# Kernel tuning notes

Hardware: AMD Instinct MI355X
Metric: run time of the kernel (lower is better)

The kernel has to match this reference:

```python
import jax, jax.numpy as jnp
import numpy as np

E = 1024  # embed_dim
H = 16    # num_heads
D = E // H  # head_dim


def setup_inputs() -> dict:
    key = jax.random.key(0)
    ks = jax.random.split(key, 9)
    s = 0.02
    return {
        "hidden_state": jax.random.normal(ks[0], (4, 1024, E), jnp.float32),
        "Wq": jax.random.normal(ks[1], (H, D, E), jnp.float32) * s,
        "bq": jax.random.normal(ks[2], (H, D), jnp.float32) * s,
        "Wk": jax.random.normal(ks[3], (H, D, E), jnp.float32) * s,
        "bk": jax.random.normal(ks[4], (H, D), jnp.float32) * s,
        "Wv": jax.random.normal(ks[5], (H, D, E), jnp.float32) * s,
        "bv": jax.random.normal(ks[6], (H, D), jnp.float32) * s,
        "Wo": jax.random.normal(ks[7], (E, E), jnp.float32) * s,
        "bo": jax.random.normal(ks[8], (E,), jnp.float32) * s,
    }


def _mha(x, Wq, bq, Wk, bk, Wv, bv, Wo, bo):
    # Per-head linear projections (torch Linear: y = x W^T + b), batched over heads.
    q = jnp.einsum("bse,hde->bhsd", x, Wq) + bq[None, :, None, :]
    k = jnp.einsum("bse,hde->bhsd", x, Wk) + bk[None, :, None, :]
    v = jnp.einsum("bse,hde->bhsd", x, Wv) + bv[None, :, None, :]
    scores = jnp.einsum("bhsd,bhtd->bhst", q, k) / jnp.sqrt(jnp.asarray(D, x.dtype))
    w = jax.nn.softmax(scores, axis=-1)  # F.softmax default -> last dim
    o = jnp.einsum("bhst,bhtd->bhsd", w, v)
    # concat heads along last dim: [B,S,H*D] in head order (matches torch.cat)
    B, _, S, _ = o.shape
    o = jnp.transpose(o, (0, 2, 1, 3)).reshape(B, S, H * D)
    return o @ Wo.T + bo


def reference(hidden_state, Wq, bq, Wk, bk, Wv, bv, Wo, bo):
    return _mha(hidden_state, Wq, bq, Wk, bk, Wv, bv, Wo, bo)
```

## Files before the change

### kernel.cpp

```cpp
#include <hip/hip_runtime.h>
#include <hip/hip_bf16.h>
#include <stdint.h>

#define E_DIM 1024
#define H_NUM 16
#define D_DIM 64
#define B_NUM 4
#define S_LEN 1024

typedef __attribute__((ext_vector_type(8))) short bf16x8;
typedef __attribute__((ext_vector_type(4))) short bf16x4;
typedef __attribute__((ext_vector_type(4))) float f32x4;

#define SOFTMAX_C2 0.18033688011112042f

__device__ inline ushort f2b(float x) {
    __hip_bfloat16 h = __float2bfloat16(x);
    return *(ushort*)&h;
}
__device__ inline float b2f(ushort u) {
    __hip_bfloat16 h = *(__hip_bfloat16*)&u;
    return __bfloat162float(h);
}
__device__ inline uint pk2(float a, float b) {
    __hip_bfloat162 h = __float22bfloat162_rn(make_float2(a, b));
    return *(uint*)&h;
}
__device__ inline float fexp2(float x) { return __builtin_amdgcn_exp2f(x); }

__device__ inline void gld16(const ushort* g, ushort* l) {
    __builtin_amdgcn_global_load_lds((const __attribute__((address_space(1))) void*)g,
                                     (__attribute__((address_space(3))) void*)l, 16, 0, 0);
}

__global__ __launch_bounds__(256)
void convert_all(const float* __restrict__ X,  const float* __restrict__ Wq,
                 const float* __restrict__ Wk, const float* __restrict__ Wv,
                 const float* __restrict__ Wo,
                 ushort* __restrict__ Xb, ushort* __restrict__ Wcat,
                 ushort* __restrict__ Wob)
{
    const int bid = blockIdx.x;
    const float* src; ushort* dst; size_t off;
    if (bid < 4096)      { src = X;  dst = Xb;   off = (size_t)bid * 1024; }
    else if (bid < 5120) { src = Wq; dst = Wcat;              off = (size_t)(bid - 4096) * 1024; }
    else if (bid < 6144) { src = Wk; dst = Wcat + (1u << 20); off = (size_t)(bid - 5120) * 1024; }
    else if (bid < 7168) { src = Wv; dst = Wcat + (2u << 20); off = (size_t)(bid - 6144) * 1024; }
    else                 { src = Wo; dst = Wob;               off = (size_t)(bid - 7168) * 1024; }
    const size_t i = off + (size_t)threadIdx.x * 4;
    float4 v = *(const float4*)&src[i];
    ushort4 o;
    o.x = f2b(v.x); o.y = f2b(v.y); o.z = f2b(v.z); o.w = f2b(v.w);
    *(ushort4*)&dst[i] = o;
}

__global__ __launch_bounds__(256, 2)
void gemm_qkv(const ushort* __restrict__ A, const ushort* __restrict__ Bw,
              const float* __restrict__ b0, const float* __restrict__ b1,
              const float* __restrict__ b2,
              ushort* __restrict__ Qb, ushort* __restrict__ Kb,
              ushort* __restrict__ Vt_g, int K)
{
    __shared__ __align__(16) ushort SM[32768];
    ushort* As = SM;
    ushort* Bs = SM + 16384;

    const int tid  = threadIdx.x;
    const int wave = tid >> 6;
    const int lane = tid & 63;
    const int quad = lane >> 4;
    const int l16  = lane & 15;
    const int wm   = wave & 1;
    const int wn   = wave >> 1;
    const int m0   = blockIdx.x * 128;
    const int n0   = blockIdx.y * 128;

    f32x4 acc[4][4] = {};

    auto stageA = [&](int buf, int k0) {
#pragma unroll
        for (int i = 0; i < 4; ++i) {
            const int e   = i * 256 + tid;
            const int row = e >> 3;
            const int gc8 = ((e & 7) ^ (row & 7)) * 8;
            gld16(&A[(size_t)(m0 + row) * K + k0 + gc8], &As[buf * 8192 + e * 8]);
        }
    };
    auto stageB = [&](int buf, int k0) {
#pragma unroll
        for (int i = 0; i < 4; ++i) {
            const int e   = i * 256 + tid;
            const int row = e >> 3;
            const int gc8 = ((e & 7) ^ (row & 7)) * 8;
            gld16(&Bw[(size_t)(n0 + row) * K + k0 + gc8], &Bs[buf * 8192 + e * 8]);
        }
    };

    stageA(0, 0); stageB(0, 0);
    __syncthreads();

    const int nk = K >> 6;
    const int xa = (l16 & 7) * 8;
    for (int ki = 0; ki < nk; ++ki) {
        const int cur = ki & 1;
        if (ki + 1 < nk) { stageA(cur ^ 1, (ki + 1) << 6); stageB(cur ^ 1, (ki + 1) << 6); }

#pragma unroll
        for (int ks = 0; ks < 2; ++ks) {
            const int lc = (ks * 32 + quad * 8) ^ xa;
            bf16x8 af[4], bf[4];
#pragma unroll
            for (int mi = 0; mi < 4; ++mi)
                af[mi] = *(const bf16x8*)&As[cur * 8192 + (wm * 64 + mi * 16 + l16) * 64 + lc];
#pragma unroll
            for (int ni = 0; ni < 4; ++ni)
                bf[ni] = *(const bf16x8*)&Bs[cur * 8192 + (wn * 64 + ni * 16 + l16) * 64 + lc];
#pragma unroll
            for (int mi = 0; mi < 4; ++mi)
#pragma unroll
                for (int ni = 0; ni < 4; ++ni)
                    acc[mi][ni] = __builtin_amdgcn_mfma_f32_16x16x32_bf16(af[mi], bf[ni], acc[mi][ni], 0, 0, 0);
        }
        __syncthreads();
    }

    const int seg   = n0 >> 10;
    const int cbase = n0 & 1023;
    const float* bp = (seg == 0) ? b0 : (seg == 1) ? b1 : b2;
    const float scl = (seg == 0) ? SOFTMAX_C2 : 1.0f;

    if (seg < 2) {
        ushort* T = SM;
#pragma unroll
        for (int ni = 0; ni < 4; ++ni) {
            const int nloc = wn * 64 + ni * 16 + l16;
            const float bv = bp[cbase + nloc];
#pragma unroll
            for (int mi = 0; mi < 4; ++mi)
#pragma unroll
                for (int r = 0; r < 4; ++r)
                    T[(wm * 64 + mi * 16 + quad * 4 + r) * 136 + nloc] =
                        f2b((acc[mi][ni][r] + bv) * scl);
        }
        __syncthreads();
        ushort* dst = (seg == 0) ? Qb : Kb;
        const int row = tid >> 1, half = tid & 1;
        const ushort* s = &T[row * 136 + half * 64];
        ushort* d = &dst[(size_t)(m0 + row) * 1024 + cbase + half * 64];
#pragma unroll
        for (int j = 0; j < 8; ++j)
            *(uint4*)(d + j * 8) = *(const uint4*)(s + j * 8);
    } else {
        ushort* Tt = SM;
        const int b  = m0 >> 10, sbase = m0 & 1023;
#pragma unroll
        for (int ni = 0; ni < 4; ++ni) {
            const int nloc = wn * 64 + ni * 16 + l16;
            const float bv = bp[cbase + nloc];
#pragma unroll
            for (int mi = 0; mi < 4; ++mi) {
                const int mloc = wm * 64 + mi * 16 + quad * 4;
                ushort4 pk;
                pk.x = f2b(acc[mi][ni][0] + bv);
                pk.y = f2b(acc[mi][ni][1] + bv);
                pk.z = f2b(acc[mi][ni][2] + bv);
                pk.w = f2b(acc[mi][ni][3] + bv);
                *(ushort4*)&Tt[nloc * 136 + mloc] = pk;
            }
        }
        __syncthreads();
        const int nrow = tid >> 1, half = tid & 1;
        const int hh   = (cbase >> 6) + (nrow >> 6);
        const int drow = nrow & 63;
        const ushort* s = &Tt[nrow * 136 + half * 64];
        ushort* d = &Vt_g[(((size_t)(b * 16 + hh)) * 64 + drow) * 1024 + sbase + half * 64];
#pragma unroll
        for (int j = 0; j < 8; ++j)
            *(uint4*)(d + j * 8) = *(const uint4*)(s + j * 8);
    }
}

__global__ __launch_bounds__(256, 8)
void attention11(const ushort* __restrict__ Qg, const ushort* __restrict__ Kg,
                 const ushort* __restrict__ Vg, ushort* __restrict__ Anorm)
{
    __shared__ __align__(16) ushort SM[9216];

    const int tid  = threadIdx.x;
    const int w    = tid >> 6;
    const int lane = tid & 63;
    const int quad = lane >> 4;
    const int l16  = lane & 15;

    const int gid = blockIdx.x;
    const int qt  = (gid >> 3) & 15;
    const int bh  = (gid & 7) | ((gid >> 7) << 3);
    const int b   = bh >> 4;
    const int h   = bh & 15;
    const size_t tbase = ((size_t)b * S_LEN) * E_DIM + (size_t)h * D_DIM;
    const size_t vbase = (size_t)bh * D_DIM * S_LEN;

    const ushort* qrow = Qg + tbase + (size_t)(qt * 64 + w * 16 + l16) * E_DIM + quad * 8;
    bf16x8 qf[2];
    qf[0] = *(const bf16x8*)qrow;
    qf[1] = *(const bf16x8*)(qrow + 32);

    const int krow = tid >> 3, kslot = tid & 7;
    const int vr   = tid >> 2, vc = (tid & 3) * 8;

    const ushort* kptr = Kg + tbase + (size_t)krow * E_DIM + ((kslot ^ (krow & 7)) * 8);
    const ushort* vptr = Vg + vbase + (size_t)vr * S_LEN + vc;

    gld16(kptr, &SM[tid * 8]);
    {
        uint4 v0 = *(const uint4*)vptr;
        *(uint4*)&SM[4096 + vr * 36 + vc] = v0;
    }
    __syncthreads();

    float lq = 0.0f;
    f32x4 oacc[4] = {};
    const int xk = (l16 & 7);

    for (int kt = 0; kt < 32; ++kt) {
        const int cur = kt & 1;

        uint4 vpre;
        if (kt < 31) {
            kptr += 32 * E_DIM;
            gld16(kptr, &SM[(cur ^ 1) * 2048 + tid * 8]);
            vptr += 32;
            vpre = *(const uint4*)vptr;
        }

        f32x4 sacc[2] = {};
#pragma unroll
        for (int mt = 0; mt < 2; ++mt)
#pragma unroll
            for (int ks = 0; ks < 2; ++ks) {
                bf16x8 kf = *(const bf16x8*)&SM[cur * 2048 + (mt * 16 + l16) * 64 +
                                                (((ks * 4 + quad) ^ xk) * 8)];
                sacc[mt] = __builtin_amdgcn_mfma_f32_16x16x32_bf16(kf, qf[ks], sacc[mt], 0, 0, 0);
            }

        bf16x4 pf[2];
        float rs = 0.0f;
#pragma unroll
        for (int mt = 0; mt < 2; ++mt) {
            float p0 = fexp2(sacc[mt][0]);
            float p1 = fexp2(sacc[mt][1]);
            float p2 = fexp2(sacc[mt][2]);
            float p3 = fexp2(sacc[mt][3]);
            rs += (p0 + p1) + (p2 + p3);
            union { uint uu[2]; bf16x4 v; } pk;
            pk.uu[0] = pk2(p0, p1);
            pk.uu[1] = pk2(p2, p3);
            pf[mt] = pk.v;
        }
        lq += rs;

#pragma unroll
        for (int nb = 0; nb < 4; ++nb)
#pragma unroll
            for (int kb = 0; kb < 2; ++kb) {
                bf16x4 vf = *(const bf16x4*)&SM[4096 + cur * 2304 +
                                                (nb * 16 + l16) * 36 + kb * 16 + quad * 4];
                oacc[nb] = __builtin_amdgcn_mfma_f32_16x16x16bf16_1k(pf[kb], vf, oacc[nb], 0, 0, 0);
            }

        if (kt < 31)
            *(uint4*)&SM[4096 + (cur ^ 1) * 2304 + vr * 36 + vc] = vpre;
        __syncthreads();
    }

    lq += __shfl_xor(lq, 16);
    lq += __shfl_xor(lq, 32);

    float linv[4];
#pragma unroll
    for (int r = 0; r < 4; ++r)
        linv[r] = __builtin_amdgcn_rcpf(__shfl(lq, quad * 4 + r));

    ushort* T = SM;
#pragma unroll
    for (int nb = 0; nb < 4; ++nb)
#pragma unroll
        for (int r = 0; r < 4; ++r)
            T[(w * 16 + quad * 4 + r) * 72 + nb * 16 + l16] = f2b(oacc[nb][r] * linv[r]);
    __syncthreads();
    {
        const int row = tid >> 2, c16 = (tid & 3) * 16;
        const ushort* s = &T[row * 72 + c16];
        ushort* d = &Anorm[(size_t)(b * 1024 + qt * 64 + row) * 1024 + h * 64 + c16];
        *(uint4*)(d)     = *(const uint4*)(s);
        *(uint4*)(d + 8) = *(const uint4*)(s + 8);
    }
}

__global__ __launch_bounds__(256, 4)
void gemm_out(const ushort* __restrict__ A, const ushort* __restrict__ Bw,
              const float* __restrict__ bias, float* __restrict__ Cout)
{
    __shared__ __align__(16) ushort SM[16384];
    ushort* As = SM;
    ushort* Bs = SM + 8192;

    const int tid  = threadIdx.x;
    const int w    = tid >> 6;
    const int lane = tid & 63;
    const int quad = lane >> 4;
    const int l16  = lane & 15;
    const int m0   = blockIdx.x * 64;
    const int n0   = blockIdx.y * 64;

    f32x4 acc[4] = {};

    auto stageA = [&](int buf, int k0) {
#pragma unroll
        for (int i = 0; i < 2; ++i) {
            const int e   = i * 256 + tid;
            const int row = e >> 3;
            const int gc8 = ((e & 7) ^ (row & 7)) * 8;
            gld16(&A[(size_t)(m0 + row) * 1024 + k0 + gc8], &As[buf * 4096 + e * 8]);
        }
    };
    auto stageB = [&](int buf, int k0) {
#pragma unroll
        for (int i = 0; i < 2; ++i) {
            const int e   = i * 256 + tid;
            const int row = e >> 3;
            const int gc8 = ((e & 7) ^ (row & 7)) * 8;
            gld16(&Bw[(size_t)(n0 + row) * 1024 + k0 + gc8], &Bs[buf * 4096 + e * 8]);
        }
    };

    stageA(0, 0); stageB(0, 0);
    __syncthreads();

    const int xa = (l16 & 7) * 8;
    for (int ki = 0; ki < 16; ++ki) {
        const int cur = ki & 1;
        if (ki + 1 < 16) { stageA(cur ^ 1, (ki + 1) << 6); stageB(cur ^ 1, (ki + 1) << 6); }

#pragma unroll
        for (int ks = 0; ks < 2; ++ks) {
            const int lc = (ks * 32 + quad * 8) ^ xa;
            bf16x8 af = *(const bf16x8*)&As[cur * 4096 + (w * 16 + l16) * 64 + lc];
#pragma unroll
            for (int nb = 0; nb < 4; ++nb) {
                bf16x8 bf = *(const bf16x8*)&Bs[cur * 4096 + (nb * 16 + l16) * 64 + lc];
                acc[nb] = __builtin_amdgcn_mfma_f32_16x16x32_bf16(af, bf, acc[nb], 0, 0, 0);
            }
        }
        __syncthreads();
    }

    float* Tf = (float*)SM;
#pragma unroll
    for (int nb = 0; nb < 4; ++nb) {
        const float bv = bias[n0 + nb * 16 + l16];
#pragma unroll
        for (int r = 0; r < 4; ++r)
            Tf[(w * 16 + quad * 4 + r) * 68 + nb * 16 + l16] = acc[nb][r] + bv;
    }
    __syncthreads();
    {
        const int row = tid >> 2, c16 = (tid & 3) * 16;
        const float* s = &Tf[row * 68 + c16];
        float* d = &Cout[(size_t)(m0 + row) * 1024 + n0 + c16];
#pragma unroll
        for (int j = 0; j < 4; ++j)
            *(float4*)(d + j * 4) = *(const float4*)(s + j * 4);
    }
}

extern "C" void kernel_launch(void* const* d_in, const int* in_sizes, int n_in,
                              void* d_out, int out_size, void* d_ws, size_t ws_size,
                              hipStream_t stream)
{
    (void)in_sizes; (void)n_in; (void)out_size; (void)ws_size;

    const float* X  = (const float*)d_in[0];
    const float* Wq = (const float*)d_in[1];
    const float* bq = (const float*)d_in[2];
    const float* Wk = (const float*)d_in[3];
    const float* bk = (const float*)d_in[4];
    const float* Wv = (const float*)d_in[5];
    const float* bv = (const float*)d_in[6];
    const float* Wo = (const float*)d_in[7];
    const float* bo = (const float*)d_in[8];

    const size_t MEG = 1u << 20;
    ushort* ws    = (ushort*)d_ws;
    ushort* Xb    = ws;
    ushort* Wcat  = ws + 4 * MEG;
    ushort* Wob   = ws + 7 * MEG;
    ushort* Qb    = ws + 8 * MEG;
    ushort* Kb    = ws + 12 * MEG;
    ushort* Vtg   = ws + 16 * MEG;
    ushort* Anorm = ws + 20 * MEG;

    dim3 blk(256);

    convert_all<<<8192, blk, 0, stream>>>(X, Wq, Wk, Wv, Wo, Xb, Wcat, Wob);

    gemm_qkv<<<dim3(32, 24), blk, 0, stream>>>(Xb, Wcat, bq, bk, bv,
                                               Qb, Kb, Vtg, E_DIM);

    attention11<<<1024, blk, 0, stream>>>(Qb, Kb, Vtg, Anorm);

    gemm_out<<<dim3(64, 16), blk, 0, stream>>>(Anorm, Wob, bo, (float*)d_out);
}
```

Before: 176.4 us.

## Shrink attention blocks to 32 queries, add MFMA priority, enlarge output GEMM tile

The attention kernel now uses 128-thread blocks covering 32 query rows, with twice as many blocks. Each thread loads two K/V chunks per tile, and s_setprio raises wave priority around the MFMA sections. The output projection GEMM moves to a 128x64 tile with a 2x2 wave layout and 4x2 MFMA sub-tiles per wave, which raises operand reuse but lowers occupancy. Smaller attention blocks spread the work across more CUs, but each block now reloads K/V for half as many queries, roughly doubling K/V traffic.

```diff
diff --git a/kernel.cpp b/kernel.cpp
--- a/kernel.cpp
+++ b/kernel.cpp
@@ -180,8 +180,8 @@
     }
 }
 
-__global__ __launch_bounds__(256, 8)
-void attention11(const ushort* __restrict__ Qg, const ushort* __restrict__ Kg,
+__global__ __launch_bounds__(128, 4)
+void attention12(const ushort* __restrict__ Qg, const ushort* __restrict__ Kg,
                  const ushort* __restrict__ Vg, ushort* __restrict__ Anorm)
 {
     __shared__ __align__(16) ushort SM[9216];
@@ -193,14 +193,14 @@
     const int l16  = lane & 15;
 
     const int gid = blockIdx.x;
-    const int qt  = (gid >> 3) & 15;
-    const int bh  = (gid & 7) | ((gid >> 7) << 3);
+    const int qt  = (gid >> 3) & 31;
+    const int bh  = (gid & 7) | ((gid >> 8) << 3);
     const int b   = bh >> 4;
     const int h   = bh & 15;
     const size_t tbase = ((size_t)b * S_LEN) * E_DIM + (size_t)h * D_DIM;
     const size_t vbase = (size_t)bh * D_DIM * S_LEN;
 
-    const ushort* qrow = Qg + tbase + (size_t)(qt * 64 + w * 16 + l16) * E_DIM + quad * 8;
+    const ushort* qrow = Qg + tbase + (size_t)(qt * 32 + w * 16 + l16) * E_DIM + quad * 8;
     bf16x8 qf[2];
     qf[0] = *(const bf16x8*)qrow;
     qf[1] = *(const bf16x8*)(qrow + 32);
@@ -211,10 +211,13 @@
     const ushort* kptr = Kg + tbase + (size_t)krow * E_DIM + ((kslot ^ (krow & 7)) * 8);
     const ushort* vptr = Vg + vbase + (size_t)vr * S_LEN + vc;
 
-    gld16(kptr, &SM[tid * 8]);
+    gld16(kptr,               &SM[tid * 8]);
+    gld16(kptr + 16 * E_DIM,  &SM[(128 + tid) * 8]);
     {
         uint4 v0 = *(const uint4*)vptr;
-        *(uint4*)&SM[4096 + vr * 36 + vc] = v0;
+        uint4 v1 = *(const uint4*)(vptr + 32 * S_LEN);
+        *(uint4*)&SM[4096 + vr * 36 + vc]        = v0;
+        *(uint4*)&SM[4096 + (vr + 32) * 36 + vc] = v1;
     }
     __syncthreads();
 
@@ -225,15 +228,18 @@
     for (int kt = 0; kt < 32; ++kt) {
         const int cur = kt & 1;
 
-        uint4 vpre;
+        uint4 vpre0, vpre1;
         if (kt < 31) {
             kptr += 32 * E_DIM;
-            gld16(kptr, &SM[(cur ^ 1) * 2048 + tid * 8]);
+            gld16(kptr,              &SM[(cur ^ 1) * 2048 + tid * 8]);
+            gld16(kptr + 16 * E_DIM, &SM[(cur ^ 1) * 2048 + (128 + tid) * 8]);
             vptr += 32;
-            vpre = *(const uint4*)vptr;
+            vpre0 = *(const uint4*)vptr;
+            vpre1 = *(const uint4*)(vptr + 32 * S_LEN);
         }
 
         f32x4 sacc[2] = {};
+        __builtin_amdgcn_s_setprio(1);
 #pragma unroll
         for (int mt = 0; mt < 2; ++mt)
 #pragma unroll
@@ -242,6 +248,7 @@
                                                 (((ks * 4 + quad) ^ xk) * 8)];
                 sacc[mt] = __builtin_amdgcn_mfma_f32_16x16x32_bf16(kf, qf[ks], sacc[mt], 0, 0, 0);
             }
+        __builtin_amdgcn_s_setprio(0);
 
         bf16x4 pf[2];
         float rs = 0.0f;
@@ -259,6 +266,7 @@
         }
         lq += rs;
 
+        __builtin_amdgcn_s_setprio(1);
 #pragma unroll
         for (int nb = 0; nb < 4; ++nb)
 #pragma unroll
@@ -267,9 +275,12 @@
                                                 (nb * 16 + l16) * 36 + kb * 16 + quad * 4];
                 oacc[nb] = __builtin_amdgcn_mfma_f32_16x16x16bf16_1k(pf[kb], vf, oacc[nb], 0, 0, 0);
             }
-
-        if (kt < 31)
-            *(uint4*)&SM[4096 + (cur ^ 1) * 2304 + vr * 36 + vc] = vpre;
+        __builtin_amdgcn_s_setprio(0);
+
+        if (kt < 31) {
+            *(uint4*)&SM[4096 + (cur ^ 1) * 2304 + vr * 36 + vc]        = vpre0;
+            *(uint4*)&SM[4096 + (cur ^ 1) * 2304 + (vr + 32) * 36 + vc] = vpre1;
+        }
         __syncthreads();
     }
 
@@ -291,37 +302,39 @@
     {
         const int row = tid >> 2, c16 = (tid & 3) * 16;
         const ushort* s = &T[row * 72 + c16];
-        ushort* d = &Anorm[(size_t)(b * 1024 + qt * 64 + row) * 1024 + h * 64 + c16];
+        ushort* d = &Anorm[(size_t)(b * 1024 + qt * 32 + row) * 1024 + h * 64 + c16];
         *(uint4*)(d)     = *(const uint4*)(s);
         *(uint4*)(d + 8) = *(const uint4*)(s + 8);
     }
 }
 
-__global__ __launch_bounds__(256, 4)
+__global__ __launch_bounds__(256, 2)
 void gemm_out(const ushort* __restrict__ A, const ushort* __restrict__ Bw,
               const float* __restrict__ bias, float* __restrict__ Cout)
 {
-    __shared__ __align__(16) ushort SM[16384];
+    __shared__ __align__(16) ushort SM[24576];
     ushort* As = SM;
-    ushort* Bs = SM + 8192;
+    ushort* Bs = SM + 16384;
 
     const int tid  = threadIdx.x;
-    const int w    = tid >> 6;
+    const int wave = tid >> 6;
     const int lane = tid & 63;
     const int quad = lane >> 4;
     const int l16  = lane & 15;
-    const int m0   = blockIdx.x * 64;
+    const int wm   = wave & 1;
+    const int wn   = wave >> 1;
+    const int m0   = blockIdx.x * 128;
     const int n0   = blockIdx.y * 64;
 
-    f32x4 acc[4] = {};
+    f32x4 acc[4][2] = {};
 
     auto stageA = [&](int buf, int k0) {
 #pragma unroll
-        for (int i = 0; i < 2; ++i) {
+        for (int i = 0; i < 4; ++i) {
             const int e   = i * 256 + tid;
             const int row = e >> 3;
             const int gc8 = ((e & 7) ^ (row & 7)) * 8;
-            gld16(&A[(size_t)(m0 + row) * 1024 + k0 + gc8], &As[buf * 4096 + e * 8]);
+            gld16(&A[(size_t)(m0 + row) * 1024 + k0 + gc8], &As[buf * 8192 + e * 8]);
         }
     };
     auto stageB = [&](int buf, int k0) {
@@ -345,31 +358,40 @@
 #pragma unroll
         for (int ks = 0; ks < 2; ++ks) {
             const int lc = (ks * 32 + quad * 8) ^ xa;
-            bf16x8 af = *(const bf16x8*)&As[cur * 4096 + (w * 16 + l16) * 64 + lc];
-#pragma unroll
-            for (int nb = 0; nb < 4; ++nb) {
-                bf16x8 bf = *(const bf16x8*)&Bs[cur * 4096 + (nb * 16 + l16) * 64 + lc];
-                acc[nb] = __builtin_amdgcn_mfma_f32_16x16x32_bf16(af, bf, acc[nb], 0, 0, 0);
-            }
+            bf16x8 af[4], bf[2];
+#pragma unroll
+            for (int mi = 0; mi < 4; ++mi)
+                af[mi] = *(const bf16x8*)&As[cur * 8192 + (wm * 64 + mi * 16 + l16) * 64 + lc];
+#pragma unroll
+            for (int ni = 0; ni < 2; ++ni)
+                bf[ni] = *(const bf16x8*)&Bs[cur * 4096 + (wn * 32 + ni * 16 + l16) * 64 + lc];
+#pragma unroll
+            for (int mi = 0; mi < 4; ++mi)
+#pragma unroll
+                for (int ni = 0; ni < 2; ++ni)
+                    acc[mi][ni] = __builtin_amdgcn_mfma_f32_16x16x32_bf16(af[mi], bf[ni], acc[mi][ni], 0, 0, 0);
         }
         __syncthreads();
     }
 
     float* Tf = (float*)SM;
 #pragma unroll
-    for (int nb = 0; nb < 4; ++nb) {
-        const float bv = bias[n0 + nb * 16 + l16];
-#pragma unroll
-        for (int r = 0; r < 4; ++r)
-            Tf[(w * 16 + quad * 4 + r) * 68 + nb * 16 + l16] = acc[nb][r] + bv;
+    for (int ni = 0; ni < 2; ++ni) {
+        const int nloc = wn * 32 + ni * 16 + l16;
+        const float bv = bias[n0 + nloc];
+#pragma unroll
+        for (int mi = 0; mi < 4; ++mi)
+#pragma unroll
+            for (int r = 0; r < 4; ++r)
+                Tf[(wm * 64 + mi * 16 + quad * 4 + r) * 68 + nloc] = acc[mi][ni][r] + bv;
     }
     __syncthreads();
     {
-        const int row = tid >> 2, c16 = (tid & 3) * 16;
-        const float* s = &Tf[row * 68 + c16];
-        float* d = &Cout[(size_t)(m0 + row) * 1024 + n0 + c16];
-#pragma unroll
-        for (int j = 0; j < 4; ++j)
+        const int row = tid >> 1, half = tid & 1;
+        const float* s = &Tf[row * 68 + half * 32];
+        float* d = &Cout[(size_t)(m0 + row) * 1024 + n0 + half * 32];
+#pragma unroll
+        for (int j = 0; j < 8; ++j)
             *(float4*)(d + j * 4) = *(const float4*)(s + j * 4);
     }
 }
@@ -407,7 +429,7 @@
     gemm_qkv<<<dim3(32, 24), blk, 0, stream>>>(Xb, Wcat, bq, bk, bv,
                                                Qb, Kb, Vtg, E_DIM);
 
-    attention11<<<1024, blk, 0, stream>>>(Qb, Kb, Vtg, Anorm);
-
-    gemm_out<<<dim3(64, 16), blk, 0, stream>>>(Anorm, Wob, bo, (float*)d_out);
-}
+    attention12<<<2048, dim3(128), 0, stream>>>(Qb, Kb, Vtg, Anorm);
+
+    gemm_out<<<dim3(32, 16), blk, 0, stream>>>(Anorm, Wob, bo, (float*)d_out);
+}
```

Result: no change. 177.1 us (+0.4%).
